# Performance work log

Hardware: AMD Instinct MI355X
Metric: run time of the kernel (lower is better)

Reference implementation:

```python
import jax, jax.numpy as jnp
import numpy as np

N_TOKENS = 32768
N_EMBED = 8192
EMBED_DIM = 512


def setup_inputs() -> dict:
    key = jax.random.key(0)
    k1, k2 = jax.random.split(key)
    xs = jax.random.normal(k1, (N_TOKENS, EMBED_DIM), dtype=jnp.float32)
    embed_weight = jax.random.normal(k2, (N_EMBED, EMBED_DIM), dtype=jnp.float32)
    return {"xs": xs, "embed_weight": embed_weight}


def reference(xs, embed_weight):
    # Squared Euclidean distance: [N, n_embed]
    distance = (
        jnp.sum(xs ** 2, axis=1, keepdims=True)
        + jnp.sum(embed_weight ** 2, axis=1)
        - 2.0 * jnp.matmul(xs, embed_weight.T)
    )
    indices = jnp.argmin(distance, axis=1)          # [N]
    output = embed_weight[indices]                  # gather: [N, embed_dim]
    # straight-through estimator
    output_x = xs + jax.lax.stop_gradient(output - xs)
    return output_x
```

## Files before the change

### kernel.cpp

```cpp
#include <hip/hip_runtime.h>


#define M_TOK 32768
#define N_EMB 8192
#define D_K   512
#define WOFF  2048.0f
#define QMASK 0xFFFFFF80u
#define BAND  5.5f
#define NT    8
#define SCALE 22.6786f
#define M2C   (-2.0f / (SCALE * SCALE))

typedef __attribute__((ext_vector_type(4))) int   i32x4;
typedef unsigned long long u64;
typedef unsigned int u32;

__device__ __forceinline__ void gload16(const void* g, void* l) {
  __builtin_amdgcn_global_load_lds(
      (const __attribute__((address_space(1))) unsigned int*)g,
      (__attribute__((address_space(3))) unsigned int*)l, 16, 0, 0);
}

__device__ __forceinline__ u32 map_f(float f) {
  u32 u = __float_as_uint(f);
  return u ^ ((u & 0x80000000u) ? 0xFFFFFFFFu : 0x80000000u);
}
__device__ __forceinline__ float qval(u32 key) {
  return __uint_as_float(key & QMASK) - WOFF;
}
__device__ __forceinline__ int q8(float x) {
  int v = __float2int_rn(x * SCALE);
  return v < -127 ? -127 : (v > 127 ? 127 : v);
}

__global__ __launch_bounds__(256) void quant_x_kernel(const float* __restrict__ src,
                                                      char* __restrict__ dst, int n16) {
  int e = blockIdx.x * 256 + threadIdx.x;
  if (e >= n16) return;
  const float4* s4 = (const float4*)src + (size_t)e * 4;
  char out[16];
  #pragma unroll
  for (int i = 0; i < 4; ++i) {
    float4 v = s4[i];
    out[i * 4 + 0] = (char)q8(v.x);
    out[i * 4 + 1] = (char)q8(v.y);
    out[i * 4 + 2] = (char)q8(v.z);
    out[i * 4 + 3] = (char)q8(v.w);
  }
  ((int4*)dst)[e] = *(const int4*)out;
}

__global__ __launch_bounds__(256) void quant_w_kernel(const float* __restrict__ w,
                                                      char* __restrict__ Wq,
                                                      float* __restrict__ wnorm) {
  const int row  = blockIdx.x * 4 + (threadIdx.x >> 6);
  const int lane = threadIdx.x & 63;
  const float4* wr = (const float4*)(w + (size_t)row * D_K);
  float4 v0 = wr[lane * 2], v1 = wr[lane * 2 + 1];
  char out[8];
  out[0] = (char)q8(v0.x); out[1] = (char)q8(v0.y);
  out[2] = (char)q8(v0.z); out[3] = (char)q8(v0.w);
  out[4] = (char)q8(v1.x); out[5] = (char)q8(v1.y);
  out[6] = (char)q8(v1.z); out[7] = (char)q8(v1.w);
  *(int2*)(Wq + (size_t)row * D_K + lane * 8) = *(const int2*)out;
  float s = v0.x*v0.x + v0.y*v0.y + v0.z*v0.z + v0.w*v0.w
          + v1.x*v1.x + v1.y*v1.y + v1.z*v1.z + v1.w*v1.w;
  #pragma unroll
  for (int off = 32; off; off >>= 1) s += __shfl_xor(s, off);
  if (lane == 0) wnorm[row] = s;
}

__global__ __launch_bounds__(256, 3) void dist_mfma_kernel(
    const char* __restrict__ Xq, const char* __restrict__ Wq,
    const float* __restrict__ wnorm, uint2* __restrict__ partials) {
  __shared__ char smem[32768];

  int bid = (int)blockIdx.x;
  const int swz = (bid & 7) * 2048 + (bid >> 3);
  const int rt = swz & 255, ct = swz >> 8;
  const int row0 = rt * 128, col0 = ct * 128;

  const int tid  = threadIdx.x;
  const int w    = tid >> 6, lane = tid & 63;
  const int wr   = w >> 1,  wc   = w & 1;
  const int g    = lane >> 4, cl = lane & 15;

  const char* gA = Xq + (size_t)row0 * D_K;
  const char* gB = Wq + (size_t)col0 * D_K;

  int srcoff[2];
  #pragma unroll
  for (int q = 0; q < 2; ++q) {
    const int c = q * 256 + tid;
    const int r = c >> 2;
    srcoff[q] = r * 512 + (((c & 3) ^ ((r >> 1) & 3)) * 16);
  }

  int offA[4], offB[4];
  #pragma unroll
  for (int m = 0; m < 4; ++m) {
    const int rl = wr * 64 + m * 16 + cl;
    offA[m] = rl * 64 + ((g ^ ((rl >> 1) & 3)) * 16);
  }
  #pragma unroll
  for (int n = 0; n < 4; ++n) {
    const int rl = wc * 64 + n * 16 + cl;
    offB[n] = 8192 + rl * 64 + ((g ^ ((rl >> 1) & 3)) * 16);
  }

  #define STG(bo, kt)                                                          \
    { _Pragma("unroll") for (int q = 0; q < 2; ++q)                            \
        gload16(gA + srcoff[q] + (kt) * 64,                                    \
                smem + (bo) + q * 4096 + w * 1024);                            \
      _Pragma("unroll") for (int q = 0; q < 2; ++q)                            \
        gload16(gB + srcoff[q] + (kt) * 64,                                    \
                smem + (bo) + 8192 + q * 4096 + w * 1024); }

  i32x4 acc[4][4];
  #pragma unroll
  for (int i = 0; i < 4; i++)
    #pragma unroll
    for (int j = 0; j < 4; j++) acc[i][j] = (i32x4)(0);

  STG(0, 0);
  __syncthreads();

  for (int t = 0; t < NT; ++t) {
    const int rb = (t & 1) * 16384, sb = rb ^ 16384;
    if (t < NT - 1) STG(sb, t + 1);

    i32x4 a[4], b[4];
    #pragma unroll
    for (int m = 0; m < 4; ++m) a[m] = *(const i32x4*)(smem + rb + offA[m]);
    #pragma unroll
    for (int n = 0; n < 4; ++n) b[n] = *(const i32x4*)(smem + rb + offB[n]);

    #pragma unroll
    for (int m = 0; m < 4; ++m)
      #pragma unroll
      for (int n = 0; n < 4; ++n)
        acc[m][n] = __builtin_amdgcn_mfma_i32_16x16x64_i8(a[m], b[n], acc[m][n], 0, 0, 0);

    __syncthreads();
  }
  #undef STG

  float wnp[4];
  u32 colb[4];
  #pragma unroll
  for (int n = 0; n < 4; ++n) {
    const int colL = wc * 64 + n * 16 + cl;
    wnp[n]  = wnorm[col0 + colL] + WOFF;
    colb[n] = (u32)colL;
  }

  uint2* cmb = (uint2*)smem;

  #pragma unroll
  for (int m = 0; m < 4; ++m) {
    #pragma unroll
    for (int r = 0; r < 4; ++r) {
      float s0 = fmaf((float)acc[m][0][r], M2C, wnp[0]);
      float s1 = fmaf((float)acc[m][1][r], M2C, wnp[1]);
      float s2 = fmaf((float)acc[m][2][r], M2C, wnp[2]);
      float s3 = fmaf((float)acc[m][3][r], M2C, wnp[3]);
      u32 k0 = (__float_as_uint(s0) & QMASK) | colb[0];
      u32 k1 = (__float_as_uint(s1) & QMASK) | colb[1];
      u32 k2 = (__float_as_uint(s2) & QMASK) | colb[2];
      u32 k3 = (__float_as_uint(s3) & QMASK) | colb[3];
      u32 pa = min(k0, k1), pb = max(k0, k1);
      u32 pc = min(k2, k3), pd = max(k2, k3);
      u32 c1 = min(pa, pc);
      u32 c2 = min(max(pa, pc), min(pb, pd));
      #pragma unroll
      for (int off = 1; off < 16; off <<= 1) {
        u32 o1 = __shfl_xor(c1, off), o2 = __shfl_xor(c2, off);
        u32 n1 = min(c1, o1);
        c2 = min(min(c2, o2), max(c1, o1));
        c1 = n1;
      }
      if (cl == 0) cmb[(wr * 64 + m * 16 + g * 4 + r) * 2 + wc] = make_uint2(c1, c2);
    }
  }
  __syncthreads();
  if (tid < 128) {
    uint2 A = cmb[tid * 2], B = cmb[tid * 2 + 1];
    u32 c1 = min(A.x, B.x);
    u32 c2 = min(max(A.x, B.x), min(A.y, B.y));
    partials[(size_t)ct * M_TOK + row0 + tid] = make_uint2(c1, c2);
  }
}

__global__ __launch_bounds__(256) void argmin_wave_kernel(
    const uint2* __restrict__ partials, const float* __restrict__ xs,
    const float* __restrict__ w, const float* __restrict__ wnorm,
    int* __restrict__ fidx) {
  const int t = blockIdx.x * 4 + (threadIdx.x >> 6);
  const int lane = threadIdx.x & 63;

  const uint2 e = partials[(size_t)lane * M_TOK + t];
  u32 b1 = e.x, b2 = e.y;
  #pragma unroll
  for (int off = 1; off < 64; off <<= 1) {
    u32 o1 = __shfl_xor(b1, off), o2 = __shfl_xor(b2, off);
    u32 n1 = min(b1, o1);
    b2 = min(min(b2, o2), max(b1, o1));
    b1 = n1;
  }
  const int bl = __ffsll(__ballot(e.x == b1)) - 1;
  const int bidx = bl * 128 + (int)(b1 & 127u);

  if (qval(b2) - qval(b1) >= BAND) {
    if (lane == 0) fidx[t] = bidx;
    return;
  }

  const float thr = qval(b1) + BAND;
  const bool in2 = qval(e.y) <= thr;
  const bool in1 = (qval(e.x) <= thr) && !in2;
  u64 mask1 = __ballot(in1);
  u64 mask2 = __ballot(in2);

  const float4* xr = (const float4*)(xs + (size_t)t * D_K);
  const float4 xv0 = xr[lane * 2], xv1 = xr[lane * 2 + 1];

  u64 best = ~0ULL;
  #define EXACT_DOT(j)                                                         \
    {                                                                          \
      const float4* wrp = (const float4*)(w + (size_t)(j) * D_K);              \
      float4 w0 = wrp[lane * 2], w1 = wrp[lane * 2 + 1];                       \
      float s = xv0.x*w0.x + xv0.y*w0.y + xv0.z*w0.z + xv0.w*w0.w              \
              + xv1.x*w1.x + xv1.y*w1.y + xv1.z*w1.z + xv1.w*w1.w;             \
      _Pragma("unroll")                                                        \
      for (int off = 32; off; off >>= 1) s += __shfl_xor(s, off);              \
      float score = wnorm[j] - 2.0f * s;                                       \
      u64 k = ((u64)map_f(score) << 32) | (u32)(j);                            \
      best = k < best ? k : best;                                              \
    }

  while (mask1) {
    const int l = __ffsll(mask1) - 1;
    mask1 &= mask1 - 1;
    const u32 key = __shfl(e.x, l);
    const int j = l * 128 + (int)(key & 127u);
    EXACT_DOT(j);
  }
  while (mask2) {
    const int l = __ffsll(mask2) - 1;
    mask2 &= mask2 - 1;
    for (int c = 0; c < 128; ++c) {
      const int j = l * 128 + c;
      EXACT_DOT(j);
    }
  }
  #undef EXACT_DOT

  if (lane == 0) fidx[t] = (int)(best & 0xFFFFFFFFULL);
}

__global__ __launch_bounds__(256) void gather_kernel(const float* __restrict__ xs,
                                                     const float* __restrict__ w,
                                                     const int* __restrict__ fidx,
                                                     float* __restrict__ out) {
  int e = blockIdx.x * 256 + threadIdx.x;
  int row = e >> 7, off = e & 127;
  float4 xv = ((const float4*)(xs + (size_t)row * D_K))[off];
  float4 wv = ((const float4*)(w  + (size_t)fidx[row] * D_K))[off];
  float4 o;
  o.x = xv.x + (wv.x - xv.x);
  o.y = xv.y + (wv.y - xv.y);
  o.z = xv.z + (wv.z - xv.z);
  o.w = xv.w + (wv.w - xv.w);
  ((float4*)out)[e] = o;
}

extern "C" void kernel_launch(void* const* d_in, const int* in_sizes, int n_in,
                              void* d_out, int out_size, void* d_ws, size_t ws_size,
                              hipStream_t stream) {
  const float* xs = (const float*)d_in[0];
  const float* w  = (const float*)d_in[1];
  float* out = (float*)d_out;

  char* p = (char*)d_ws;
  char*  Xq       = p;                       p += (size_t)M_TOK * D_K;
  char*  Wq       = p;                       p += (size_t)N_EMB * D_K;
  float* wnorm    = (float*)p;               p += (size_t)N_EMB * 4;
  uint2* partials = (uint2*)p;               p += (size_t)64 * M_TOK * 8;
  int*   fidx     = (int*)p;

  quant_x_kernel<<<(M_TOK * D_K / 16) / 256, 256, 0, stream>>>(xs, Xq, M_TOK * D_K / 16);
  quant_w_kernel<<<N_EMB / 4, 256, 0, stream>>>(w, Wq, wnorm);
  dist_mfma_kernel<<<(M_TOK / 128) * (N_EMB / 128), 256, 0, stream>>>(Xq, Wq, wnorm, partials);
  argmin_wave_kernel<<<M_TOK / 4, 256, 0, stream>>>(partials, xs, w, wnorm, fidx);
  gather_kernel<<<(M_TOK * (D_K / 4)) / 256, 256, 0, stream>>>(xs, w, fidx, out);
}
```

Baseline: 363.5 us.

## Fuse argmin refinement with gather and transpose partials to row-major

```diff
diff --git a/kernel.cpp b/kernel.cpp
--- a/kernel.cpp
+++ b/kernel.cpp
@@ -187,18 +187,18 @@
     uint2 A = cmb[tid * 2], B = cmb[tid * 2 + 1];
     u32 c1 = min(A.x, B.x);
     u32 c2 = min(max(A.x, B.x), min(A.y, B.y));
-    partials[(size_t)ct * M_TOK + row0 + tid] = make_uint2(c1, c2);
-  }
-}
-
-__global__ __launch_bounds__(256) void argmin_wave_kernel(
+    partials[(size_t)(row0 + tid) * 64 + ct] = make_uint2(c1, c2);
+  }
+}
+
+__global__ __launch_bounds__(256) void argmin_gather_kernel(
     const uint2* __restrict__ partials, const float* __restrict__ xs,
     const float* __restrict__ w, const float* __restrict__ wnorm,
-    int* __restrict__ fidx) {
+    float* __restrict__ out) {
   const int t = blockIdx.x * 4 + (threadIdx.x >> 6);
   const int lane = threadIdx.x & 63;
 
-  const uint2 e = partials[(size_t)lane * M_TOK + t];
+  const uint2 e = partials[(size_t)t * 64 + lane];
   u32 b1 = e.x, b2 = e.y;
   #pragma unroll
   for (int off = 1; off < 64; off <<= 1) {
@@ -208,70 +208,61 @@
     b1 = n1;
   }
   const int bl = __ffsll(__ballot(e.x == b1)) - 1;
-  const int bidx = bl * 128 + (int)(b1 & 127u);
-
-  if (qval(b2) - qval(b1) >= BAND) {
-    if (lane == 0) fidx[t] = bidx;
-    return;
-  }
-
-  const float thr = qval(b1) + BAND;
-  const bool in2 = qval(e.y) <= thr;
-  const bool in1 = (qval(e.x) <= thr) && !in2;
-  u64 mask1 = __ballot(in1);
-  u64 mask2 = __ballot(in2);
+  int idx = bl * 128 + (int)(b1 & 127u);
 
   const float4* xr = (const float4*)(xs + (size_t)t * D_K);
   const float4 xv0 = xr[lane * 2], xv1 = xr[lane * 2 + 1];
 
-  u64 best = ~0ULL;
-  #define EXACT_DOT(j)                                                         \
-    {                                                                          \
-      const float4* wrp = (const float4*)(w + (size_t)(j) * D_K);              \
-      float4 w0 = wrp[lane * 2], w1 = wrp[lane * 2 + 1];                       \
-      float s = xv0.x*w0.x + xv0.y*w0.y + xv0.z*w0.z + xv0.w*w0.w              \
-              + xv1.x*w1.x + xv1.y*w1.y + xv1.z*w1.z + xv1.w*w1.w;             \
-      _Pragma("unroll")                                                        \
-      for (int off = 32; off; off >>= 1) s += __shfl_xor(s, off);              \
-      float score = wnorm[j] - 2.0f * s;                                       \
-      u64 k = ((u64)map_f(score) << 32) | (u32)(j);                            \
-      best = k < best ? k : best;                                              \
-    }
-
-  while (mask1) {
-    const int l = __ffsll(mask1) - 1;
-    mask1 &= mask1 - 1;
-    const u32 key = __shfl(e.x, l);
-    const int j = l * 128 + (int)(key & 127u);
-    EXACT_DOT(j);
-  }
-  while (mask2) {
-    const int l = __ffsll(mask2) - 1;
-    mask2 &= mask2 - 1;
-    for (int c = 0; c < 128; ++c) {
-      const int j = l * 128 + c;
+  if (qval(b2) - qval(b1) < BAND) {
+    const float thr = qval(b1) + BAND;
+    const bool in2 = qval(e.y) <= thr;
+    const bool in1 = (qval(e.x) <= thr) && !in2;
+    u64 mask1 = __ballot(in1);
+    u64 mask2 = __ballot(in2);
+
+    u64 best = ~0ULL;
+    #define EXACT_DOT(j)                                                       \
+      {                                                                        \
+        const float4* wrp = (const float4*)(w + (size_t)(j) * D_K);            \
+        float4 w0 = wrp[lane * 2], w1 = wrp[lane * 2 + 1];                     \
+        float s = xv0.x*w0.x + xv0.y*w0.y + xv0.z*w0.z + xv0.w*w0.w            \
+                + xv1.x*w1.x + xv1.y*w1.y + xv1.z*w1.z + xv1.w*w1.w;           \
+        _Pragma("unroll")                                                      \
+        for (int off = 32; off; off >>= 1) s += __shfl_xor(s, off);            \
+        float score = wnorm[j] - 2.0f * s;                                     \
+        u64 k = ((u64)map_f(score) << 32) | (u32)(j);                          \
+        best = k < best ? k : best;                                           \
+      }
+
+    while (mask1) {
+      const int l = __ffsll(mask1) - 1;
+      mask1 &= mask1 - 1;
+      const u32 key = __shfl(e.x, l);
+      const int j = l * 128 + (int)(key & 127u);
       EXACT_DOT(j);
     }
-  }
-  #undef EXACT_DOT
-
-  if (lane == 0) fidx[t] = (int)(best & 0xFFFFFFFFULL);
-}
-
-__global__ __launch_bounds__(256) void gather_kernel(const float* __restrict__ xs,
-                                                     const float* __restrict__ w,
-                                                     const int* __restrict__ fidx,
-                                                     float* __restrict__ out) {
-  int e = blockIdx.x * 256 + threadIdx.x;
-  int row = e >> 7, off = e & 127;
-  float4 xv = ((const float4*)(xs + (size_t)row * D_K))[off];
-  float4 wv = ((const float4*)(w  + (size_t)fidx[row] * D_K))[off];
-  float4 o;
-  o.x = xv.x + (wv.x - xv.x);
-  o.y = xv.y + (wv.y - xv.y);
-  o.z = xv.z + (wv.z - xv.z);
-  o.w = xv.w + (wv.w - xv.w);
-  ((float4*)out)[e] = o;
+    while (mask2) {
+      const int l = __ffsll(mask2) - 1;
+      mask2 &= mask2 - 1;
+      for (int c = 0; c < 128; ++c) {
+        const int j = l * 128 + c;
+        EXACT_DOT(j);
+      }
+    }
+    #undef EXACT_DOT
+    idx = (int)(best & 0xFFFFFFFFULL);
+  }
+
+  const float4* wrp = (const float4*)(w + (size_t)idx * D_K);
+  float4 w0 = wrp[lane * 2], w1 = wrp[lane * 2 + 1];
+  float4 o0, o1;
+  o0.x = xv0.x + (w0.x - xv0.x); o0.y = xv0.y + (w0.y - xv0.y);
+  o0.z = xv0.z + (w0.z - xv0.z); o0.w = xv0.w + (w0.w - xv0.w);
+  o1.x = xv1.x + (w1.x - xv1.x); o1.y = xv1.y + (w1.y - xv1.y);
+  o1.z = xv1.z + (w1.z - xv1.z); o1.w = xv1.w + (w1.w - xv1.w);
+  float4* orow = (float4*)(out + (size_t)t * D_K);
+  orow[lane * 2]     = o0;
+  orow[lane * 2 + 1] = o1;
 }
 
 extern "C" void kernel_launch(void* const* d_in, const int* in_sizes, int n_in,
@@ -285,12 +276,10 @@
   char*  Xq       = p;                       p += (size_t)M_TOK * D_K;
   char*  Wq       = p;                       p += (size_t)N_EMB * D_K;
   float* wnorm    = (float*)p;               p += (size_t)N_EMB * 4;
-  uint2* partials = (uint2*)p;               p += (size_t)64 * M_TOK * 8;
-  int*   fidx     = (int*)p;
+  uint2* partials = (uint2*)p;
 
   quant_x_kernel<<<(M_TOK * D_K / 16) / 256, 256, 0, stream>>>(xs, Xq, M_TOK * D_K / 16);
   quant_w_kernel<<<N_EMB / 4, 256, 0, stream>>>(w, Wq, wnorm);
   dist_mfma_kernel<<<(M_TOK / 128) * (N_EMB / 128), 256, 0, stream>>>(Xq, Wq, wnorm, partials);
-  argmin_wave_kernel<<<M_TOK / 4, 256, 0, stream>>>(partials, xs, w, wnorm, fidx);
-  gather_kernel<<<(M_TOK * (D_K / 4)) / 256, 256, 0, stream>>>(xs, w, fidx, out);
-}
+  argmin_gather_kernel<<<M_TOK / 4, 256, 0, stream>>>(partials, xs, w, wnorm, out);
+}
```

After: 347.0 us (median of 2 runs). 1.05x faster.
